# Performance work log

Measured on AMD Instinct MI355X. Metric: run time of the kernel, lower is better.

Reference implementation:

```python
import jax, jax.numpy as jnp
import numpy as np

B, N, A, M, D = 64, 128, 64, 128, 64  # batch, in_caps, in_dim, out_caps, out_dim
SCALE = 1.0 / np.sqrt(D).astype(np.float32)
W_INIT = np.sqrt(M / (A * N)).astype(np.float32)


def setup_inputs() -> dict:
    key = jax.random.key(0)
    k1, k2, k3, k4, k5 = jax.random.split(key, 5)
    return {
        "input": jax.random.normal(k1, (B, N, A), dtype=jnp.float32),
        "current_act": jax.random.uniform(k2, (B, N), dtype=jnp.float32),
        "next_capsule_value": jax.random.normal(k3, (B, M, D), dtype=jnp.float32),
        "next_act": jax.random.uniform(k4, (B, M), dtype=jnp.float32),
        "w": W_INIT * jax.random.normal(k5, (N, A, M, D), dtype=jnp.float32),
        "num_iter": 1,
    }


def reference(input, current_act, next_capsule_value, next_act, w, num_iter):
    # Per-(input-capsule, output-capsule) votes: bna,namd->bnmd (shared by both einsums)
    votes = jnp.einsum('bna,namd->bnmd', input, w)
    # Routing logits: agreement between votes and current output poses
    logits = jnp.einsum('bnmd,bmd->bnm', votes, next_capsule_value) * SCALE
    qk = jax.nn.softmax(logits, axis=2)
    # Modulate by next-layer activations and renormalize over output capsules
    qk = qk * next_act[:, None, :]
    qk = qk / (jnp.sum(qk, axis=2, keepdims=True) + 1e-10)
    # Weighted aggregation of votes, gated by input-capsule activations
    ncv = jnp.einsum('bnm,bnmd,bn->bmd', qk, votes, current_act)
    # act_type == 'ONES'; dropout rate 0.0 (identity); nonlinear_act is identity
    na = jnp.ones(ncv.shape[:2], dtype=ncv.dtype)
    return ncv, na, qk
```

## Files before the change

kernel.cpp:

```cpp
#include <hip/hip_runtime.h>

typedef __attribute__((ext_vector_type(8))) short bf16x8;
typedef __attribute__((ext_vector_type(4))) float f32x4;

constexpr int Bq = 64, Nq = 128, Aq = 64, Mq = 128, Dq = 64;
constexpr int MD = Mq * Dq;
constexpr int NM = Nq * Mq;
constexpr int NA = Nq * Aq;
constexpr int NCV_SZ = Bq * MD;
constexpr int NA_SZ  = Bq * Mq;
constexpr float SCALE = 0.125f;

__device__ __forceinline__ unsigned short f2b(float f) {
  unsigned u = __float_as_uint(f);
  return (unsigned short)((u + 0x7fffu + ((u >> 16) & 1u)) >> 16);
}
__device__ __forceinline__ unsigned cvt2(float lo, float hi) {
  return ((unsigned)f2b(hi) << 16) | (unsigned)f2b(lo);
}
__device__ __forceinline__ bf16x8 pack8(const float* v) {
  union { unsigned u[4]; bf16x8 b; } x;
  x.u[0] = cvt2(v[0], v[1]); x.u[1] = cvt2(v[2], v[3]);
  x.u[2] = cvt2(v[4], v[5]); x.u[3] = cvt2(v[6], v[7]);
  return x.b;
}
__device__ __forceinline__ void dma16(const float* g, float* l) {
  __builtin_amdgcn_global_load_lds(
      (const __attribute__((address_space(1))) unsigned*)g,
      (__attribute__((address_space(3))) unsigned*)l, 16, 0, 0);
}

__global__ __launch_bounds__(256) void k0_init(float* __restrict__ out) {
  int i = blockIdx.x * 256 + threadIdx.x;
  if (i < NCV_SZ) out[i] = 0.0f;
  else if (i < NCV_SZ + NA_SZ) out[i] = 1.0f;
}

__global__ __launch_bounds__(256, 2) void k1_logits(
    const float* __restrict__ input,
    const float* __restrict__ ncvin,
    const float* __restrict__ wgt,
    float* __restrict__ logits) {
  const int mc = blockIdx.x;
  const int n0 = blockIdx.y * 8;
  const int t  = threadIdx.x;
  const int wv = t >> 6, l = t & 63;
  const int lr = l & 15, g = l >> 4;
  const int m  = mc * 4 + wv;

  __shared__ float Wf[2][32 * 256];

  float cnv[4][4][4];
#pragma unroll
  for (int i = 0; i < 4; ++i)
#pragma unroll
    for (int j = 0; j < 4; ++j)
#pragma unroll
      for (int r = 0; r < 4; ++r)
        cnv[i][j][r] = ncvin[(size_t)(16 * i + 4 * g + r) * MD + m * Dq + 16 * j + lr];

  auto stage = [&](int h) {
    const int hh = 15 - h;
    const int nn = n0 + (hh >> 1);
    const int ks = (hh & 1) * 32;
    float* dst = &Wf[h & 1][0];
#pragma unroll
    for (int rr = 0; rr < 8; ++rr) {
      const int al = wv * 8 + rr;
      const char* gs = (const char*)(wgt + (size_t)(nn * Aq + ks + al) * MD + mc * 256)
                       + ((l * 16) ^ (((al >> 3) & 1) << 6));
      dma16((const float*)gs, dst + al * 256);
    }
  };

  stage(0);
  f32x4 acc[4][4];

  for (int h = 0; h < 16; ++h) {
    const int hh = 15 - h;
    const int nn = n0 + (hh >> 1);
    const int ks = (hh & 1) * 32;

    float av[4][8];
#pragma unroll
    for (int i = 0; i < 4; ++i) {
      const float* ap = input + (size_t)(16 * i + lr) * NA + nn * Aq + ks + g * 8;
      *(float4*)&av[i][0] = *(const float4*)ap;
      *(float4*)&av[i][4] = *(const float4*)(ap + 4);
    }
    __builtin_amdgcn_sched_barrier(0);

    if (h < 15) {
      stage(h + 1);
      asm volatile("s_waitcnt vmcnt(8)" ::: "memory");
    } else {
      asm volatile("s_waitcnt vmcnt(0)" ::: "memory");
    }
    __builtin_amdgcn_s_barrier();

    if ((h & 1) == 0) {
#pragma unroll
      for (int i = 0; i < 4; ++i)
#pragma unroll
        for (int j = 0; j < 4; ++j) acc[i][j] = (f32x4)(0.0f);
    }

    bf16x8 af[4];
#pragma unroll
    for (int i = 0; i < 4; ++i) af[i] = pack8(av[i]);

    const float* bufp = &Wf[h & 1][0];
#pragma unroll
    for (int j = 0; j < 4; ++j) {
      const int c  = 64 * wv + 16 * j + lr;
      const int cx = c ^ ((g & 1) << 4);
      float bv[8];
#pragma unroll
      for (int e = 0; e < 8; ++e) bv[e] = bufp[(g * 8 + e) * 256 + cx];
      bf16x8 bf = pack8(bv);
#pragma unroll
      for (int i = 0; i < 4; ++i)
        acc[i][j] = __builtin_amdgcn_mfma_f32_16x16x32_bf16(af[i], bf, acc[i][j], 0, 0, 0);
    }
    __builtin_amdgcn_s_barrier();

    if (h & 1) {
      float lp[4][4];
#pragma unroll
      for (int i = 0; i < 4; ++i)
#pragma unroll
        for (int r = 0; r < 4; ++r) lp[i][r] = 0.0f;
#pragma unroll
      for (int i = 0; i < 4; ++i)
#pragma unroll
        for (int j = 0; j < 4; ++j)
#pragma unroll
          for (int r = 0; r < 4; ++r)
            lp[i][r] = fmaf(acc[i][j][r], cnv[i][j][r], lp[i][r]);
#pragma unroll
      for (int off = 1; off < 16; off <<= 1)
#pragma unroll
        for (int i = 0; i < 4; ++i)
#pragma unroll
          for (int r = 0; r < 4; ++r) lp[i][r] += __shfl_xor(lp[i][r], off);
      float ov = lp[0][0];
#pragma unroll
      for (int i = 0; i < 4; ++i)
#pragma unroll
        for (int r = 0; r < 4; ++r)
          ov = (lr == i * 4 + r) ? lp[i][r] : ov;
      const int b = 16 * (lr >> 2) + 4 * g + (lr & 3);
      logits[(size_t)b * NM + (size_t)nn * Mq + m] = SCALE * ov;
    }
  }
}

__global__ __launch_bounds__(256) void k2_softmax(
    const float* __restrict__ next_act,
    float* __restrict__ qk) {
  const int row  = blockIdx.x * 4 + (threadIdx.x >> 6);
  const int lane = threadIdx.x & 63;
  const int b = row >> 7;
  float* p = qk + (size_t)row * Mq;
  float x0 = p[lane], x1 = p[lane + 64];
  float mx = fmaxf(x0, x1);
#pragma unroll
  for (int off = 32; off; off >>= 1) mx = fmaxf(mx, __shfl_xor(mx, off));
  float e0 = __expf(x0 - mx), e1 = __expf(x1 - mx);
  float s = e0 + e1;
#pragma unroll
  for (int off = 32; off; off >>= 1) s += __shfl_xor(s, off);
  float a0 = next_act[b * Mq + lane], a1 = next_act[b * Mq + lane + 64];
  float t0 = (e0 / s) * a0, t1 = (e1 / s) * a1;
  float s2 = t0 + t1;
#pragma unroll
  for (int off = 32; off; off >>= 1) s2 += __shfl_xor(s2, off);
  s2 += 1e-10f;
  p[lane]      = t0 / s2;
  p[lane + 64] = t1 / s2;
}

__global__ __launch_bounds__(256, 2) void k3_aggregate(
    const float* __restrict__ input,
    const float* __restrict__ cur_act,
    const float* __restrict__ wgt,
    const float* __restrict__ qk,
    float* __restrict__ ncv) {
  const int mc = blockIdx.x;
  const int n0 = blockIdx.y * 8;
  const int t  = threadIdx.x;
  const int wv = t >> 6, l = t & 63;
  const int lr = l & 15, g = l >> 4;
  const int m  = mc * 4 + wv;

  __shared__ float Wf[2][32 * 256];
  __shared__ float zl[8][4][64];

#pragma unroll
  for (int p = 0; p < 2; ++p) {
    const int idx = t + p * 256;
    const int b = idx >> 3, nn = idx & 7;
    float4 q4 = *(const float4*)&qk[(size_t)b * NM + (size_t)(n0 + nn) * Mq + mc * 4];
    float ca = cur_act[b * Nq + n0 + nn];
    zl[nn][0][b] = q4.x * ca; zl[nn][1][b] = q4.y * ca;
    zl[nn][2][b] = q4.z * ca; zl[nn][3][b] = q4.w * ca;
  }
  __syncthreads();

  auto stage = [&](int h) {
    const int nn = n0 + (h >> 1);
    const int ks = (h & 1) * 32;
    float* dst = &Wf[h & 1][0];
#pragma unroll
    for (int rr = 0; rr < 8; ++rr) {
      const int al = wv * 8 + rr;
      const char* gs = (const char*)(wgt + (size_t)(nn * Aq + ks + al) * MD + mc * 256)
                       + ((l * 16) ^ (((al >> 3) & 1) << 6));
      dma16((const float*)gs, dst + al * 256);
    }
  };

  stage(0);
  f32x4 acc[4][4];
#pragma unroll
  for (int i = 0; i < 4; ++i)
#pragma unroll
    for (int j = 0; j < 4; ++j) acc[i][j] = (f32x4)(0.0f);

  float zr[4];
  for (int h = 0; h < 16; ++h) {
    const int nnl = h >> 1;
    const int nn  = n0 + nnl;
    const int ks  = (h & 1) * 32;

    if ((h & 1) == 0) {
#pragma unroll
      for (int i = 0; i < 4; ++i) zr[i] = zl[nnl][wv][16 * i + lr];
    }

    float av[4][8];
#pragma unroll
    for (int i = 0; i < 4; ++i) {
      const float* ap = input + (size_t)(16 * i + lr) * NA + nn * Aq + ks + g * 8;
      *(float4*)&av[i][0] = *(const float4*)ap;
      *(float4*)&av[i][4] = *(const float4*)(ap + 4);
    }
    __builtin_amdgcn_sched_barrier(0);

    if (h < 15) {
      stage(h + 1);
      asm volatile("s_waitcnt vmcnt(8)" ::: "memory");
    } else {
      asm volatile("s_waitcnt vmcnt(0)" ::: "memory");
    }
    __builtin_amdgcn_s_barrier();

    bf16x8 af[4];
#pragma unroll
    for (int i = 0; i < 4; ++i) {
      float sv[8];
#pragma unroll
      for (int e = 0; e < 8; ++e) sv[e] = av[i][e] * zr[i];
      af[i] = pack8(sv);
    }

    const float* bufp = &Wf[h & 1][0];
#pragma unroll
    for (int j = 0; j < 4; ++j) {
      const int c  = 64 * wv + 16 * j + lr;
      const int cx = c ^ ((g & 1) << 4);
      float bv[8];
#pragma unroll
      for (int e = 0; e < 8; ++e) bv[e] = bufp[(g * 8 + e) * 256 + cx];
      bf16x8 bf = pack8(bv);
#pragma unroll
      for (int i = 0; i < 4; ++i)
        acc[i][j] = __builtin_amdgcn_mfma_f32_16x16x32_bf16(af[i], bf, acc[i][j], 0, 0, 0);
    }
    __builtin_amdgcn_s_barrier();
  }

#pragma unroll
  for (int i = 0; i < 4; ++i)
#pragma unroll
    for (int j = 0; j < 4; ++j) {
      const int d = 16 * j + lr;
#pragma unroll
      for (int r = 0; r < 4; ++r) {
        const int b = 16 * i + 4 * g + r;
        atomicAdd(&ncv[(size_t)b * MD + m * Dq + d], acc[i][j][r]);
      }
    }
}

extern "C" void kernel_launch(void* const* d_in, const int* in_sizes, int n_in,
                              void* d_out, int out_size, void* d_ws, size_t ws_size,
                              hipStream_t stream) {
  const float* input    = (const float*)d_in[0];
  const float* cur_act  = (const float*)d_in[1];
  const float* ncvin    = (const float*)d_in[2];
  const float* next_act = (const float*)d_in[3];
  const float* wgt      = (const float*)d_in[4];

  float* out = (float*)d_out;
  float* ncv = out;
  float* qk  = out + NCV_SZ + NA_SZ;

  k0_init<<<(NCV_SZ + NA_SZ + 255) / 256, 256, 0, stream>>>(out);
  k1_logits<<<dim3(32, 16), 256, 0, stream>>>(input, ncvin, wgt, qk);
  k2_softmax<<<(Bq * Nq) / 4, 256, 0, stream>>>(next_act, qk);
  k3_aggregate<<<dim3(32, 16), 256, 0, stream>>>(input, cur_act, wgt, qk, ncv);
}
```

Measured before the change: 161.3 us.

## Pre-convert weights to bf16 MFMA fragment layout in workspace before logits and aggregation

Adds a conversion kernel that repacks the fp32 weight tensor into bf16 in the exact per-lane MFMA B-fragment order inside the workspace. The logits and aggregation kernels then stage half as many bytes per tile and load fragments directly from LDS, with no per-element packing. This removes LDS gather and conversion work in the two GEMM kernels but adds a full extra read of the weights plus a write of the bf16 copy every call. The old kernels are kept as a fallback when the workspace is too small.

After: 207.2 us. +28.4%, slower.

```diff
diff --git a/kernel.cpp b/kernel.cpp
--- a/kernel.cpp
+++ b/kernel.cpp
@@ -10,6 +10,7 @@
 constexpr int NCV_SZ = Bq * MD;
 constexpr int NA_SZ  = Bq * Mq;
 constexpr float SCALE = 0.125f;
+constexpr size_t W2_BYTES = (size_t)32 * 128 * 2 * 4 * 4 * 64 * 16;
 
 __device__ __forceinline__ unsigned short f2b(float f) {
   unsigned u = __float_as_uint(f);
@@ -29,6 +30,15 @@
       (const __attribute__((address_space(1))) unsigned*)g,
       (__attribute__((address_space(3))) unsigned*)l, 16, 0, 0);
 }
+__device__ __forceinline__ void dma16c(const char* g, void* l) {
+  __builtin_amdgcn_global_load_lds(
+      (const __attribute__((address_space(1))) unsigned*)g,
+      (__attribute__((address_space(3))) unsigned*)l, 16, 0, 0);
+}
+
+__device__ __forceinline__ size_t w2base(int mc, int nn, int ks, int wv, int j) {
+  return (((((size_t)(mc * 128 + nn) * 2 + ks) * 4 + wv) * 4 + j) * 64) * 16;
+}
 
 __global__ __launch_bounds__(256) void k0_init(float* __restrict__ out) {
   int i = blockIdx.x * 256 + threadIdx.x;
@@ -36,19 +46,72 @@
   else if (i < NCV_SZ + NA_SZ) out[i] = 1.0f;
 }
 
-__global__ __launch_bounds__(256, 2) void k1_logits(
+__global__ __launch_bounds__(256) void k_conv(const float* __restrict__ wgt,
+                                              char* __restrict__ w2) {
+  const int n = blockIdx.x, oct = blockIdx.y;
+  const int ks = oct >> 2, lhi = oct & 3;
+  const int a0 = ks * 32 + lhi * 8;
+  const int t = threadIdx.x;
+  const int wv = t >> 6, l = t & 63;
+
+  __shared__ float Ls[2][8][1024];
+
+  auto stage = [&](int cg) {
+    float* dst = &Ls[cg & 1][0][0];
+#pragma unroll
+    for (int rr = 0; rr < 2; ++rr) {
+      const int e = wv * 2 + rr;
+      const float* src = wgt + ((size_t)(n * 64 + a0 + e)) * MD + cg * 1024;
+#pragma unroll
+      for (int q = 0; q < 4; ++q)
+        dma16(src + q * 256 + l * 4, dst + e * 1024 + q * 256);
+    }
+  };
+
+  stage(0);
+  for (int cg = 0; cg < 8; ++cg) {
+    if (cg < 7) {
+      stage(cg + 1);
+      asm volatile("s_waitcnt vmcnt(8)" ::: "memory");
+    } else {
+      asm volatile("s_waitcnt vmcnt(0)" ::: "memory");
+    }
+    __builtin_amdgcn_s_barrier();
+
+    const float* lsc = &Ls[cg & 1][0][0];
+    float4 tv[8];
+#pragma unroll
+    for (int e = 0; e < 8; ++e)
+      tv[e] = *(const float4*)(lsc + e * 1024 + t * 4);
+
+    const int c0 = cg * 1024 + t * 4;
+#pragma unroll
+    for (int cc = 0; cc < 4; ++cc) {
+      const int c = c0 + cc;
+      const int m = c >> 6, d = c & 63;
+      float v[8];
+#pragma unroll
+      for (int e = 0; e < 8; ++e) v[e] = ((const float*)&tv[e])[cc];
+      *(bf16x8*)(w2 + w2base(m >> 2, n, ks, m & 3, d >> 4) +
+                 (size_t)(lhi * 16 + (d & 15)) * 16) = pack8(v);
+    }
+    __builtin_amdgcn_s_barrier();
+  }
+}
+
+__global__ __launch_bounds__(256, 2) void k1_logits2(
     const float* __restrict__ input,
     const float* __restrict__ ncvin,
-    const float* __restrict__ wgt,
+    const char* __restrict__ w2,
     float* __restrict__ logits) {
   const int mc = blockIdx.x;
   const int n0 = blockIdx.y * 8;
-  const int t  = threadIdx.x;
+  const int t = threadIdx.x;
   const int wv = t >> 6, l = t & 63;
   const int lr = l & 15, g = l >> 4;
-  const int m  = mc * 4 + wv;
-
-  __shared__ float Wf[2][32 * 256];
+  const int m = mc * 4 + wv;
+
+  __shared__ uint4 Wl[2][1024];
 
   float cnv[4][4][4];
 #pragma unroll
@@ -60,31 +123,23 @@
         cnv[i][j][r] = ncvin[(size_t)(16 * i + 4 * g + r) * MD + m * Dq + 16 * j + lr];
 
   auto stage = [&](int h) {
-    const int hh = 15 - h;
-    const int nn = n0 + (hh >> 1);
-    const int ks = (hh & 1) * 32;
-    float* dst = &Wf[h & 1][0];
-#pragma unroll
-    for (int rr = 0; rr < 8; ++rr) {
-      const int al = wv * 8 + rr;
-      const char* gs = (const char*)(wgt + (size_t)(nn * Aq + ks + al) * MD + mc * 256)
-                       + ((l * 16) ^ (((al >> 3) & 1) << 6));
-      dma16((const float*)gs, dst + al * 256);
-    }
+    const int nn = n0 + (h >> 1), ks = h & 1;
+#pragma unroll
+    for (int j = 0; j < 4; ++j)
+      dma16c((const char*)w2 + w2base(mc, nn, ks, wv, j) + (size_t)l * 16,
+             &Wl[h & 1][(wv * 4 + j) * 64]);
   };
 
   stage(0);
   f32x4 acc[4][4];
 
   for (int h = 0; h < 16; ++h) {
-    const int hh = 15 - h;
-    const int nn = n0 + (hh >> 1);
-    const int ks = (hh & 1) * 32;
+    const int nn = n0 + (h >> 1), ksq = h & 1;
 
     float av[4][8];
 #pragma unroll
     for (int i = 0; i < 4; ++i) {
-      const float* ap = input + (size_t)(16 * i + lr) * NA + nn * Aq + ks + g * 8;
+      const float* ap = input + (size_t)(16 * i + lr) * NA + nn * Aq + ksq * 32 + g * 8;
       *(float4*)&av[i][0] = *(const float4*)ap;
       *(float4*)&av[i][4] = *(const float4*)(ap + 4);
     }
@@ -92,13 +147,13 @@
 
     if (h < 15) {
       stage(h + 1);
-      asm volatile("s_waitcnt vmcnt(8)" ::: "memory");
+      asm volatile("s_waitcnt vmcnt(4)" ::: "memory");
     } else {
       asm volatile("s_waitcnt vmcnt(0)" ::: "memory");
     }
     __builtin_amdgcn_s_barrier();
 
-    if ((h & 1) == 0) {
+    if (ksq == 0) {
 #pragma unroll
       for (int i = 0; i < 4; ++i)
 #pragma unroll
@@ -109,22 +164,16 @@
 #pragma unroll
     for (int i = 0; i < 4; ++i) af[i] = pack8(av[i]);
 
-    const float* bufp = &Wf[h & 1][0];
 #pragma unroll
     for (int j = 0; j < 4; ++j) {
-      const int c  = 64 * wv + 16 * j + lr;
-      const int cx = c ^ ((g & 1) << 4);
-      float bv[8];
-#pragma unroll
-      for (int e = 0; e < 8; ++e) bv[e] = bufp[(g * 8 + e) * 256 + cx];
-      bf16x8 bf = pack8(bv);
+      bf16x8 bf = *(const bf16x8*)&Wl[h & 1][(wv * 4 + j) * 64 + l];
 #pragma unroll
       for (int i = 0; i < 4; ++i)
         acc[i][j] = __builtin_amdgcn_mfma_f32_16x16x32_bf16(af[i], bf, acc[i][j], 0, 0, 0);
     }
     __builtin_amdgcn_s_barrier();
 
-    if (h & 1) {
+    if (ksq == 1) {
       float lp[4][4];
 #pragma unroll
       for (int i = 0; i < 4; ++i)
@@ -180,20 +229,20 @@
   p[lane + 64] = t1 / s2;
 }
 
-__global__ __launch_bounds__(256, 2) void k3_aggregate(
+__global__ __launch_bounds__(256, 2) void k3_aggregate2(
     const float* __restrict__ input,
     const float* __restrict__ cur_act,
-    const float* __restrict__ wgt,
+    const char* __restrict__ w2,
     const float* __restrict__ qk,
     float* __restrict__ ncv) {
   const int mc = blockIdx.x;
   const int n0 = blockIdx.y * 8;
-  const int t  = threadIdx.x;
+  const int t = threadIdx.x;
   const int wv = t >> 6, l = t & 63;
   const int lr = l & 15, g = l >> 4;
-  const int m  = mc * 4 + wv;
-
-  __shared__ float Wf[2][32 * 256];
+  const int m = mc * 4 + wv;
+
+  __shared__ uint4 Wl[2][1024];
   __shared__ float zl[8][4][64];
 
 #pragma unroll
@@ -208,8 +257,101 @@
   __syncthreads();
 
   auto stage = [&](int h) {
-    const int nn = n0 + (h >> 1);
-    const int ks = (h & 1) * 32;
+    const int nn = n0 + (h >> 1), ks = h & 1;
+#pragma unroll
+    for (int j = 0; j < 4; ++j)
+      dma16c((const char*)w2 + w2base(mc, nn, ks, wv, j) + (size_t)l * 16,
+             &Wl[h & 1][(wv * 4 + j) * 64]);
+  };
+
+  stage(0);
+  f32x4 acc[4][4];
+#pragma unroll
+  for (int i = 0; i < 4; ++i)
+#pragma unroll
+    for (int j = 0; j < 4; ++j) acc[i][j] = (f32x4)(0.0f);
+
+  float zr[4];
+  for (int h = 0; h < 16; ++h) {
+    const int nnl = h >> 1;
+    const int nn = n0 + nnl, ksq = h & 1;
+
+    if (ksq == 0) {
+#pragma unroll
+      for (int i = 0; i < 4; ++i) zr[i] = zl[nnl][wv][16 * i + lr];
+    }
+
+    float av[4][8];
+#pragma unroll
+    for (int i = 0; i < 4; ++i) {
+      const float* ap = input + (size_t)(16 * i + lr) * NA + nn * Aq + ksq * 32 + g * 8;
+      *(float4*)&av[i][0] = *(const float4*)ap;
+      *(float4*)&av[i][4] = *(const float4*)(ap + 4);
+    }
+    __builtin_amdgcn_sched_barrier(0);
+
+    if (h < 15) {
+      stage(h + 1);
+      asm volatile("s_waitcnt vmcnt(4)" ::: "memory");
+    } else {
+      asm volatile("s_waitcnt vmcnt(0)" ::: "memory");
+    }
+    __builtin_amdgcn_s_barrier();
+
+    bf16x8 af[4];
+#pragma unroll
+    for (int i = 0; i < 4; ++i) {
+      float sv[8];
+#pragma unroll
+      for (int e = 0; e < 8; ++e) sv[e] = av[i][e] * zr[i];
+      af[i] = pack8(sv);
+    }
+
+#pragma unroll
+    for (int j = 0; j < 4; ++j) {
+      bf16x8 bf = *(const bf16x8*)&Wl[h & 1][(wv * 4 + j) * 64 + l];
+#pragma unroll
+      for (int i = 0; i < 4; ++i)
+        acc[i][j] = __builtin_amdgcn_mfma_f32_16x16x32_bf16(af[i], bf, acc[i][j], 0, 0, 0);
+    }
+    __builtin_amdgcn_s_barrier();
+  }
+
+#pragma unroll
+  for (int i = 0; i < 4; ++i)
+#pragma unroll
+    for (int j = 0; j < 4; ++j) {
+      const int d = 16 * j + lr;
+#pragma unroll
+      for (int r = 0; r < 4; ++r) {
+        const int b = 16 * i + 4 * g + r;
+        atomicAdd(&ncv[(size_t)b * MD + m * Dq + d], acc[i][j][r]);
+      }
+    }
+}
+
+__global__ __launch_bounds__(256, 2) void k1_legacy(
+    const float* __restrict__ input, const float* __restrict__ ncvin,
+    const float* __restrict__ wgt, float* __restrict__ logits) {
+  const int mc = blockIdx.x;
+  const int n0 = blockIdx.y * 8;
+  const int t = threadIdx.x;
+  const int wv = t >> 6, l = t & 63;
+  const int lr = l & 15, g = l >> 4;
+  const int m = mc * 4 + wv;
+  __shared__ float Wf[2][32 * 256];
+  float cnv[4][4][4];
+#pragma unroll
+  for (int i = 0; i < 4; ++i)
+#pragma unroll
+    for (int j = 0; j < 4; ++j)
+#pragma unroll
+      for (int r = 0; r < 4; ++r)
+        cnv[i][j][r] = ncvin[(size_t)(16 * i + 4 * g + r) * MD + m * Dq + 16 * j + lr];
+  auto stage = [&](int h) {
+    const int hh = 15 - h;
+    const int nn = n0 + (hh >> 1);
+    const int ks = (hh & 1) * 32;
     float* dst = &Wf[h & 1][0];
 #pragma unroll
     for (int rr = 0; rr < 8; ++rr) {
@@ -219,25 +361,12 @@
       dma16((const float*)gs, dst + al * 256);
     }
   };
-
   stage(0);
   f32x4 acc[4][4];
-#pragma unroll
-  for (int i = 0; i < 4; ++i)
-#pragma unroll
-    for (int j = 0; j < 4; ++j) acc[i][j] = (f32x4)(0.0f);
-
-  float zr[4];
   for (int h = 0; h < 16; ++h) {
-    const int nnl = h >> 1;
-    const int nn  = n0 + nnl;
-    const int ks  = (h & 1) * 32;
-
-    if ((h & 1) == 0) {
-#pragma unroll
-      for (int i = 0; i < 4; ++i) zr[i] = zl[nnl][wv][16 * i + lr];
-    }
-
+    const int hh = 15 - h;
+    const int nn = n0 + (hh >> 1);
+    const int ks = (hh & 1) * 32;
     float av[4][8];
 #pragma unroll
     for (int i = 0; i < 4; ++i) {
@@ -246,15 +375,122 @@
       *(float4*)&av[i][4] = *(const float4*)(ap + 4);
     }
     __builtin_amdgcn_sched_barrier(0);
-
-    if (h < 15) {
-      stage(h + 1);
-      asm volatile("s_waitcnt vmcnt(8)" ::: "memory");
-    } else {
-      asm volatile("s_waitcnt vmcnt(0)" ::: "memory");
-    }
-    __builtin_amdgcn_s_barrier();
-
+    if (h < 15) { stage(h + 1); asm volatile("s_waitcnt vmcnt(8)" ::: "memory"); }
+    else { asm volatile("s_waitcnt vmcnt(0)" ::: "memory"); }
+    __builtin_amdgcn_s_barrier();
+    if ((h & 1) == 0) {
+#pragma unroll
+      for (int i = 0; i < 4; ++i)
+#pragma unroll
+        for (int j = 0; j < 4; ++j) acc[i][j] = (f32x4)(0.0f);
+    }
+    bf16x8 af[4];
+#pragma unroll
+    for (int i = 0; i < 4; ++i) af[i] = pack8(av[i]);
+    const float* bufp = &Wf[h & 1][0];
+#pragma unroll
+    for (int j = 0; j < 4; ++j) {
+      const int cx = (64 * wv + 16 * j + lr) ^ ((g & 1) << 4);
+      float bv[8];
+#pragma unroll
+      for (int e = 0; e < 8; ++e) bv[e] = bufp[(g * 8 + e) * 256 + cx];
+      bf16x8 bf = pack8(bv);
+#pragma unroll
+      for (int i = 0; i < 4; ++i)
+        acc[i][j] = __builtin_amdgcn_mfma_f32_16x16x32_bf16(af[i], bf, acc[i][j], 0, 0, 0);
+    }
+    __builtin_amdgcn_s_barrier();
+    if (h & 1) {
+      float lp[4][4];
+#pragma unroll
+      for (int i = 0; i < 4; ++i)
+#pragma unroll
+        for (int r = 0; r < 4; ++r) lp[i][r] = 0.0f;
+#pragma unroll
+      for (int i = 0; i < 4; ++i)
+#pragma unroll
+        for (int j = 0; j < 4; ++j)
+#pragma unroll
+          for (int r = 0; r < 4; ++r)
+            lp[i][r] = fmaf(acc[i][j][r], cnv[i][j][r], lp[i][r]);
+#pragma unroll
+      for (int off = 1; off < 16; off <<= 1)
+#pragma unroll
+        for (int i = 0; i < 4; ++i)
+#pragma unroll
+          for (int r = 0; r < 4; ++r) lp[i][r] += __shfl_xor(lp[i][r], off);
+      float ov = lp[0][0];
+#pragma unroll
+      for (int i = 0; i < 4; ++i)
+#pragma unroll
+        for (int r = 0; r < 4; ++r)
+          ov = (lr == i * 4 + r) ? lp[i][r] : ov;
+      const int b = 16 * (lr >> 2) + 4 * g + (lr & 3);
+      logits[(size_t)b * NM + (size_t)nn * Mq + m] = SCALE * ov;
+    }
+  }
+}
+
+__global__ __launch_bounds__(256, 2) void k3_legacy(
+    const float* __restrict__ input, const float* __restrict__ cur_act,
+    const float* __restrict__ wgt, const float* __restrict__ qk,
+    float* __restrict__ ncv) {
+  const int mc = blockIdx.x;
+  const int n0 = blockIdx.y * 8;
+  const int t = threadIdx.x;
+  const int wv = t >> 6, l = t & 63;
+  const int lr = l & 15, g = l >> 4;
+  const int m = mc * 4 + wv;
+  __shared__ float Wf[2][32 * 256];
+  __shared__ float zl[8][4][64];
+#pragma unroll
+  for (int p = 0; p < 2; ++p) {
+    const int idx = t + p * 256;
+    const int b = idx >> 3, nn = idx & 7;
+    float4 q4 = *(const float4*)&qk[(size_t)b * NM + (size_t)(n0 + nn) * Mq + mc * 4];
+    float ca = cur_act[b * Nq + n0 + nn];
+    zl[nn][0][b] = q4.x * ca; zl[nn][1][b] = q4.y * ca;
+    zl[nn][2][b] = q4.z * ca; zl[nn][3][b] = q4.w * ca;
+  }
+  __syncthreads();
+  auto stage = [&](int h) {
+    const int nn = n0 + (h >> 1);
+    const int ks = (h & 1) * 32;
+    float* dst = &Wf[h & 1][0];
+#pragma unroll
+    for (int rr = 0; rr < 8; ++rr) {
+      const int al = wv * 8 + rr;
+      const char* gs = (const char*)(wgt + (size_t)(nn * Aq + ks + al) * MD + mc * 256)
+                       + ((l * 16) ^ (((al >> 3) & 1) << 6));
+      dma16((const float*)gs, dst + al * 256);
+    }
+  };
+  stage(0);
+  f32x4 acc[4][4];
+#pragma unroll
+  for (int i = 0; i < 4; ++i)
+#pragma unroll
+    for (int j = 0; j < 4; ++j) acc[i][j] = (f32x4)(0.0f);
+  float zr[4];
+  for (int h = 0; h < 16; ++h) {
+    const int nnl = h >> 1;
+    const int nn = n0 + nnl;
+    const int ks = (h & 1) * 32;
+    if ((h & 1) == 0) {
+#pragma unroll
+      for (int i = 0; i < 4; ++i) zr[i] = zl[nnl][wv][16 * i + lr];
+    }
+    float av[4][8];
+#pragma unroll
+    for (int i = 0; i < 4; ++i) {
+      const float* ap = input + (size_t)(16 * i + lr) * NA + nn * Aq + ks + g * 8;
+      *(float4*)&av[i][0] = *(const float4*)ap;
+      *(float4*)&av[i][4] = *(const float4*)(ap + 4);
+    }
+    __builtin_amdgcn_sched_barrier(0);
+    if (h < 15) { stage(h + 1); asm volatile("s_waitcnt vmcnt(8)" ::: "memory"); }
+    else { asm volatile("s_waitcnt vmcnt(0)" ::: "memory"); }
+    __builtin_amdgcn_s_barrier();
     bf16x8 af[4];
 #pragma unroll
     for (int i = 0; i < 4; ++i) {
@@ -263,12 +499,10 @@
       for (int e = 0; e < 8; ++e) sv[e] = av[i][e] * zr[i];
       af[i] = pack8(sv);
     }
-
     const float* bufp = &Wf[h & 1][0];
 #pragma unroll
     for (int j = 0; j < 4; ++j) {
-      const int c  = 64 * wv + 16 * j + lr;
-      const int cx = c ^ ((g & 1) << 4);
+      const int cx = (64 * wv + 16 * j + lr) ^ ((g & 1) << 4);
       float bv[8];
 #pragma unroll
       for (int e = 0; e < 8; ++e) bv[e] = bufp[(g * 8 + e) * 256 + cx];
@@ -279,7 +513,6 @@
     }
     __builtin_amdgcn_s_barrier();
   }
-
 #pragma unroll
   for (int i = 0; i < 4; ++i)
 #pragma unroll
@@ -306,8 +539,17 @@
   float* ncv = out;
   float* qk  = out + NCV_SZ + NA_SZ;
 
-  k0_init<<<(NCV_SZ + NA_SZ + 255) / 256, 256, 0, stream>>>(out);
-  k1_logits<<<dim3(32, 16), 256, 0, stream>>>(input, ncvin, wgt, qk);
-  k2_softmax<<<(Bq * Nq) / 4, 256, 0, stream>>>(next_act, qk);
-  k3_aggregate<<<dim3(32, 16), 256, 0, stream>>>(input, cur_act, wgt, qk, ncv);
-}
+  if (ws_size >= W2_BYTES) {
+    char* w2 = (char*)d_ws;
+    k_conv<<<dim3(Nq, 8), 256, 0, stream>>>(wgt, w2);
+    k0_init<<<(NCV_SZ + NA_SZ + 255) / 256, 256, 0, stream>>>(out);
+    k1_logits2<<<dim3(32, 16), 256, 0, stream>>>(input, ncvin, w2, qk);
+    k2_softmax<<<(Bq * Nq) / 4, 256, 0, stream>>>(next_act, qk);
+    k3_aggregate2<<<dim3(32, 16), 256, 0, stream>>>(input, cur_act, w2, qk, ncv);
+  } else {
+    k0_init<<<(NCV_SZ + NA_SZ + 255) / 256, 256, 0, stream>>>(out);
+    k1_legacy<<<dim3(32, 16), 256, 0, stream>>>(input, ncvin, wgt, qk);
+    k2_softmax<<<(Bq * Nq) / 4, 256, 0, stream>>>(next_act, qk);
+    k3_legacy<<<dim3(32, 16), 256, 0, stream>>>(input, cur_act, wgt, qk, ncv);
+  }
+}
```

## Split batch across two wave groups with 512-thread blocks in logits and aggregate

Applied to the files above, without the earlier changes.

Both GEMM-style kernels now launch 512 threads per block, with eight waves arranged as four along the output capsule and two along the batch. Each wave holds half the accumulators, and each of the eight waves stages four W rows instead of eight. The aim is more waves per CU to hide latency, with fewer registers per thread. In exchange, each wave repeats the LDS reads and bf16 packing of W, and the logits shuffle reduction stores only half its lanes.

Measured after the change: 153.0 us. -5.1%, faster.

```diff
diff --git a/kernel.cpp b/kernel.cpp
--- a/kernel.cpp
+++ b/kernel.cpp
@@ -36,28 +36,26 @@
   else if (i < NCV_SZ + NA_SZ) out[i] = 1.0f;
 }
 
-__global__ __launch_bounds__(256, 2) void k1_logits(
-    const float* __restrict__ input,
-    const float* __restrict__ ncvin,
-    const float* __restrict__ wgt,
-    float* __restrict__ logits) {
+__global__ __launch_bounds__(512, 4) void k1_logits(
+    const float* __restrict__ input, const float* __restrict__ ncvin,
+    const float* __restrict__ wgt, float* __restrict__ logits) {
   const int mc = blockIdx.x;
   const int n0 = blockIdx.y * 8;
-  const int t  = threadIdx.x;
-  const int wv = t >> 6, l = t & 63;
+  const int t = threadIdx.x;
+  const int w8 = t >> 6, l = t & 63;
+  const int wv_m = w8 & 3, wv_b = w8 >> 2;
   const int lr = l & 15, g = l >> 4;
-  const int m  = mc * 4 + wv;
-
+  const int m = mc * 4 + wv_m;
   __shared__ float Wf[2][32 * 256];
 
-  float cnv[4][4][4];
-#pragma unroll
-  for (int i = 0; i < 4; ++i)
+  float cnv[2][4][4];
+#pragma unroll
+  for (int i = 0; i < 2; ++i)
 #pragma unroll
     for (int j = 0; j < 4; ++j)
 #pragma unroll
       for (int r = 0; r < 4; ++r)
-        cnv[i][j][r] = ncvin[(size_t)(16 * i + 4 * g + r) * MD + m * Dq + 16 * j + lr];
+        cnv[i][j][r] = ncvin[(size_t)(32 * wv_b + 16 * i + 4 * g + r) * MD + m * Dq + 16 * j + lr];
 
   auto stage = [&](int h) {
     const int hh = 15 - h;
@@ -65,26 +63,25 @@
     const int ks = (hh & 1) * 32;
     float* dst = &Wf[h & 1][0];
 #pragma unroll
-    for (int rr = 0; rr < 8; ++rr) {
-      const int al = wv * 8 + rr;
+    for (int rr = 0; rr < 4; ++rr) {
+      const int al = w8 * 4 + rr;
       const char* gs = (const char*)(wgt + (size_t)(nn * Aq + ks + al) * MD + mc * 256)
                        + ((l * 16) ^ (((al >> 3) & 1) << 6));
       dma16((const float*)gs, dst + al * 256);
     }
   };
-
   stage(0);
-  f32x4 acc[4][4];
+  f32x4 acc[2][4];
 
   for (int h = 0; h < 16; ++h) {
     const int hh = 15 - h;
     const int nn = n0 + (hh >> 1);
     const int ks = (hh & 1) * 32;
 
-    float av[4][8];
-#pragma unroll
-    for (int i = 0; i < 4; ++i) {
-      const float* ap = input + (size_t)(16 * i + lr) * NA + nn * Aq + ks + g * 8;
+    float av[2][8];
+#pragma unroll
+    for (int i = 0; i < 2; ++i) {
+      const float* ap = input + (size_t)(32 * wv_b + 16 * i + lr) * NA + nn * Aq + ks + g * 8;
       *(float4*)&av[i][0] = *(const float4*)ap;
       *(float4*)&av[i][4] = *(const float4*)(ap + 4);
     }
@@ -92,7 +89,7 @@
 
     if (h < 15) {
       stage(h + 1);
-      asm volatile("s_waitcnt vmcnt(8)" ::: "memory");
+      asm volatile("s_waitcnt vmcnt(4)" ::: "memory");
     } else {
       asm volatile("s_waitcnt vmcnt(0)" ::: "memory");
     }
@@ -100,38 +97,37 @@
 
     if ((h & 1) == 0) {
 #pragma unroll
-      for (int i = 0; i < 4; ++i)
+      for (int i = 0; i < 2; ++i)
 #pragma unroll
         for (int j = 0; j < 4; ++j) acc[i][j] = (f32x4)(0.0f);
     }
 
-    bf16x8 af[4];
-#pragma unroll
-    for (int i = 0; i < 4; ++i) af[i] = pack8(av[i]);
+    bf16x8 af[2];
+#pragma unroll
+    for (int i = 0; i < 2; ++i) af[i] = pack8(av[i]);
 
     const float* bufp = &Wf[h & 1][0];
 #pragma unroll
     for (int j = 0; j < 4; ++j) {
-      const int c  = 64 * wv + 16 * j + lr;
-      const int cx = c ^ ((g & 1) << 4);
+      const int cx = (64 * wv_m + 16 * j + lr) ^ ((g & 1) << 4);
       float bv[8];
 #pragma unroll
       for (int e = 0; e < 8; ++e) bv[e] = bufp[(g * 8 + e) * 256 + cx];
       bf16x8 bf = pack8(bv);
 #pragma unroll
-      for (int i = 0; i < 4; ++i)
+      for (int i = 0; i < 2; ++i)
         acc[i][j] = __builtin_amdgcn_mfma_f32_16x16x32_bf16(af[i], bf, acc[i][j], 0, 0, 0);
     }
     __builtin_amdgcn_s_barrier();
 
     if (h & 1) {
-      float lp[4][4];
-#pragma unroll
-      for (int i = 0; i < 4; ++i)
+      float lp[2][4];
+#pragma unroll
+      for (int i = 0; i < 2; ++i)
 #pragma unroll
         for (int r = 0; r < 4; ++r) lp[i][r] = 0.0f;
 #pragma unroll
-      for (int i = 0; i < 4; ++i)
+      for (int i = 0; i < 2; ++i)
 #pragma unroll
         for (int j = 0; j < 4; ++j)
 #pragma unroll
@@ -140,24 +136,25 @@
 #pragma unroll
       for (int off = 1; off < 16; off <<= 1)
 #pragma unroll
-        for (int i = 0; i < 4; ++i)
+        for (int i = 0; i < 2; ++i)
 #pragma unroll
           for (int r = 0; r < 4; ++r) lp[i][r] += __shfl_xor(lp[i][r], off);
       float ov = lp[0][0];
 #pragma unroll
-      for (int i = 0; i < 4; ++i)
+      for (int i = 0; i < 2; ++i)
 #pragma unroll
         for (int r = 0; r < 4; ++r)
           ov = (lr == i * 4 + r) ? lp[i][r] : ov;
-      const int b = 16 * (lr >> 2) + 4 * g + (lr & 3);
-      logits[(size_t)b * NM + (size_t)nn * Mq + m] = SCALE * ov;
+      if (lr < 8) {
+        const int b = 32 * wv_b + 16 * (lr >> 2) + 4 * g + (lr & 3);
+        logits[(size_t)b * NM + (size_t)nn * Mq + m] = SCALE * ov;
+      }
     }
   }
 }
 
 __global__ __launch_bounds__(256) void k2_softmax(
-    const float* __restrict__ next_act,
-    float* __restrict__ qk) {
+    const float* __restrict__ next_act, float* __restrict__ qk) {
   const int row  = blockIdx.x * 4 + (threadIdx.x >> 6);
   const int lane = threadIdx.x & 63;
   const int b = row >> 7;
@@ -180,26 +177,22 @@
   p[lane + 64] = t1 / s2;
 }
 
-__global__ __launch_bounds__(256, 2) void k3_aggregate(
-    const float* __restrict__ input,
-    const float* __restrict__ cur_act,
-    const float* __restrict__ wgt,
-    const float* __restrict__ qk,
+__global__ __launch_bounds__(512, 4) void k3_aggregate(
+    const float* __restrict__ input, const float* __restrict__ cur_act,
+    const float* __restrict__ wgt, const float* __restrict__ qk,
     float* __restrict__ ncv) {
   const int mc = blockIdx.x;
   const int n0 = blockIdx.y * 8;
-  const int t  = threadIdx.x;
-  const int wv = t >> 6, l = t & 63;
+  const int t = threadIdx.x;
+  const int w8 = t >> 6, l = t & 63;
+  const int wv_m = w8 & 3, wv_b = w8 >> 2;
   const int lr = l & 15, g = l >> 4;
-  const int m  = mc * 4 + wv;
-
+  const int m = mc * 4 + wv_m;
   __shared__ float Wf[2][32 * 256];
   __shared__ float zl[8][4][64];
 
-#pragma unroll
-  for (int p = 0; p < 2; ++p) {
-    const int idx = t + p * 256;
-    const int b = idx >> 3, nn = idx & 7;
+  {
+    const int b = t >> 3, nn = t & 7;
     float4 q4 = *(const float4*)&qk[(size_t)b * NM + (size_t)(n0 + nn) * Mq + mc * 4];
     float ca = cur_act[b * Nq + n0 + nn];
     zl[nn][0][b] = q4.x * ca; zl[nn][1][b] = q4.y * ca;
@@ -212,36 +205,35 @@
     const int ks = (h & 1) * 32;
     float* dst = &Wf[h & 1][0];
 #pragma unroll
-    for (int rr = 0; rr < 8; ++rr) {
-      const int al = wv * 8 + rr;
+    for (int rr = 0; rr < 4; ++rr) {
+      const int al = w8 * 4 + rr;
       const char* gs = (const char*)(wgt + (size_t)(nn * Aq + ks + al) * MD + mc * 256)
                        + ((l * 16) ^ (((al >> 3) & 1) << 6));
       dma16((const float*)gs, dst + al * 256);
     }
   };
-
   stage(0);
-  f32x4 acc[4][4];
-#pragma unroll
-  for (int i = 0; i < 4; ++i)
+  f32x4 acc[2][4];
+#pragma unroll
+  for (int i = 0; i < 2; ++i)
 #pragma unroll
     for (int j = 0; j < 4; ++j) acc[i][j] = (f32x4)(0.0f);
 
-  float zr[4];
+  float zr[2];
   for (int h = 0; h < 16; ++h) {
     const int nnl = h >> 1;
-    const int nn  = n0 + nnl;
-    const int ks  = (h & 1) * 32;
+    const int nn = n0 + nnl;
+    const int ks = (h & 1) * 32;
 
     if ((h & 1) == 0) {
 #pragma unroll
-      for (int i = 0; i < 4; ++i) zr[i] = zl[nnl][wv][16 * i + lr];
-    }
-
-    float av[4][8];
-#pragma unroll
-    for (int i = 0; i < 4; ++i) {
-      const float* ap = input + (size_t)(16 * i + lr) * NA + nn * Aq + ks + g * 8;
+      for (int i = 0; i < 2; ++i) zr[i] = zl[nnl][wv_m][32 * wv_b + 16 * i + lr];
+    }
+
+    float av[2][8];
+#pragma unroll
+    for (int i = 0; i < 2; ++i) {
+      const float* ap = input + (size_t)(32 * wv_b + 16 * i + lr) * NA + nn * Aq + ks + g * 8;
       *(float4*)&av[i][0] = *(const float4*)ap;
       *(float4*)&av[i][4] = *(const float4*)(ap + 4);
     }
@@ -249,15 +241,15 @@
 
     if (h < 15) {
       stage(h + 1);
-      asm volatile("s_waitcnt vmcnt(8)" ::: "memory");
+      asm volatile("s_waitcnt vmcnt(4)" ::: "memory");
     } else {
       asm volatile("s_waitcnt vmcnt(0)" ::: "memory");
     }
     __builtin_amdgcn_s_barrier();
 
-    bf16x8 af[4];
-#pragma unroll
-    for (int i = 0; i < 4; ++i) {
+    bf16x8 af[2];
+#pragma unroll
+    for (int i = 0; i < 2; ++i) {
       float sv[8];
 #pragma unroll
       for (int e = 0; e < 8; ++e) sv[e] = av[i][e] * zr[i];
@@ -267,27 +259,26 @@
     const float* bufp = &Wf[h & 1][0];
 #pragma unroll
     for (int j = 0; j < 4; ++j) {
-      const int c  = 64 * wv + 16 * j + lr;
-      const int cx = c ^ ((g & 1) << 4);
+      const int cx = (64 * wv_m + 16 * j + lr) ^ ((g & 1) << 4);
       float bv[8];
 #pragma unroll
       for (int e = 0; e < 8; ++e) bv[e] = bufp[(g * 8 + e) * 256 + cx];
       bf16x8 bf = pack8(bv);
 #pragma unroll
-      for (int i = 0; i < 4; ++i)
+      for (int i = 0; i < 2; ++i)
         acc[i][j] = __builtin_amdgcn_mfma_f32_16x16x32_bf16(af[i], bf, acc[i][j], 0, 0, 0);
     }
     __builtin_amdgcn_s_barrier();
   }
 
 #pragma unroll
-  for (int i = 0; i < 4; ++i)
+  for (int i = 0; i < 2; ++i)
 #pragma unroll
     for (int j = 0; j < 4; ++j) {
       const int d = 16 * j + lr;
 #pragma unroll
       for (int r = 0; r < 4; ++r) {
-        const int b = 16 * i + 4 * g + r;
+        const int b = 32 * wv_b + 16 * i + 4 * g + r;
         atomicAdd(&ncv[(size_t)b * MD + m * Dq + d], acc[i][j][r]);
       }
     }
@@ -307,7 +298,7 @@
   float* qk  = out + NCV_SZ + NA_SZ;
 
   k0_init<<<(NCV_SZ + NA_SZ + 255) / 256, 256, 0, stream>>>(out);
-  k1_logits<<<dim3(32, 16), 256, 0, stream>>>(input, ncvin, wgt, qk);
+  k1_logits<<<dim3(32, 16), 512, 0, stream>>>(input, ncvin, wgt, qk);
   k2_softmax<<<(Bq * Nq) / 4, 256, 0, stream>>>(next_act, qk);
-  k3_aggregate<<<dim3(32, 16), 256, 0, stream>>>(input, cur_act, wgt, qk, ncv);
-}
+  k3_aggregate<<<dim3(32, 16), 512, 0, stream>>>(input, cur_act, wgt, qk, ncv);
+}
```

## Give each wave a private weight LDS region and drop block barriers

Applied to the files above, without the earlier changes.

The shared LDS weight tile is split into per-wave regions. Each wave now DMA-loads only the weight slice for its own output capsule, so the two s_barrier calls per iteration in both the logits and aggregate kernels can be removed. The wait counts are adjusted so the next stage's loads stay in flight during compute. This trades block-wide synchronization for wave-local ordering, which relies on vmcnt covering the LDS DMA correctly, and it changes the global access pattern per wave.

Result: faster. 144.5 us (median of 2 runs) (-10.4%).

```diff
diff --git a/kernel.cpp b/kernel.cpp
--- a/kernel.cpp
+++ b/kernel.cpp
@@ -36,19 +36,17 @@
   else if (i < NCV_SZ + NA_SZ) out[i] = 1.0f;
 }
 
+
 __global__ __launch_bounds__(256, 2) void k1_logits(
-    const float* __restrict__ input,
-    const float* __restrict__ ncvin,
-    const float* __restrict__ wgt,
-    float* __restrict__ logits) {
+    const float* __restrict__ input, const float* __restrict__ ncvin,
+    const float* __restrict__ wgt, float* __restrict__ logits) {
   const int mc = blockIdx.x;
   const int n0 = blockIdx.y * 8;
-  const int t  = threadIdx.x;
+  const int t = threadIdx.x;
   const int wv = t >> 6, l = t & 63;
   const int lr = l & 15, g = l >> 4;
-  const int m  = mc * 4 + wv;
-
-  __shared__ float Wf[2][32 * 256];
+  const int m = mc * 4 + wv;
+  __shared__ float Wr[4][2][2048];
 
   float cnv[4][4][4];
 #pragma unroll
@@ -59,44 +57,42 @@
       for (int r = 0; r < 4; ++r)
         cnv[i][j][r] = ncvin[(size_t)(16 * i + 4 * g + r) * MD + m * Dq + 16 * j + lr];
 
-  auto stage = [&](int h) {
+  auto stageH = [&](int h) {
+    if (h > 15) return;
     const int hh = 15 - h;
-    const int nn = n0 + (hh >> 1);
-    const int ks = (hh & 1) * 32;
-    float* dst = &Wf[h & 1][0];
-#pragma unroll
-    for (int rr = 0; rr < 8; ++rr) {
-      const int al = wv * 8 + rr;
-      const char* gs = (const char*)(wgt + (size_t)(nn * Aq + ks + al) * MD + mc * 256)
-                       + ((l * 16) ^ (((al >> 3) & 1) << 6));
-      dma16((const float*)gs, dst + al * 256);
+    const int nn = n0 + (hh >> 1), ks = hh & 1;
+    char* dst = (char*)&Wr[wv][h & 1][0];
+    const char* wb = (const char*)wgt;
+#pragma unroll
+    for (int al = 0; al < 8; ++al) {
+      const int swz = (al >> 1) & 1;
+      const char* gs = wb + (size_t)(nn * 64 + ks * 32 + al * 4 + g) * 32768
+                       + (size_t)m * 256 + ((lr * 16) ^ (swz << 6));
+      dma16((const float*)gs, (float*)(dst + al * 1024));
     }
   };
-
-  stage(0);
-  f32x4 acc[4][4];
-
-  for (int h = 0; h < 16; ++h) {
+  auto loadAv = [&](int h, float (&av)[4][8]) {
     const int hh = 15 - h;
-    const int nn = n0 + (hh >> 1);
-    const int ks = (hh & 1) * 32;
-
-    float av[4][8];
+    const int nn = n0 + (hh >> 1), ks = hh & 1;
 #pragma unroll
     for (int i = 0; i < 4; ++i) {
-      const float* ap = input + (size_t)(16 * i + lr) * NA + nn * Aq + ks + g * 8;
+      const float* ap = input + (size_t)(16 * i + lr) * NA + nn * Aq + ks * 32 + g * 8;
       *(float4*)&av[i][0] = *(const float4*)ap;
       *(float4*)&av[i][4] = *(const float4*)(ap + 4);
     }
-    __builtin_amdgcn_sched_barrier(0);
-
-    if (h < 15) {
-      stage(h + 1);
-      asm volatile("s_waitcnt vmcnt(8)" ::: "memory");
-    } else {
-      asm volatile("s_waitcnt vmcnt(0)" ::: "memory");
-    }
-    __builtin_amdgcn_s_barrier();
+  };
+
+  stageH(0);
+  f32x4 acc[4][4];
+  for (int h = 0; h < 16; ++h) {
+    float av[4][8];
+    loadAv(h, av);
+    __builtin_amdgcn_sched_barrier(0);
+    stageH(h + 1);
+    __builtin_amdgcn_sched_barrier(0);
+    if (h < 15) asm volatile("s_waitcnt vmcnt(16)" ::: "memory");
+    else        asm volatile("s_waitcnt vmcnt(8)"  ::: "memory");
+    __builtin_amdgcn_sched_barrier(0);
 
     if ((h & 1) == 0) {
 #pragma unroll
@@ -109,22 +105,21 @@
 #pragma unroll
     for (int i = 0; i < 4; ++i) af[i] = pack8(av[i]);
 
-    const float* bufp = &Wf[h & 1][0];
+    const char* lb = (const char*)&Wr[wv][h & 1][0];
 #pragma unroll
     for (int j = 0; j < 4; ++j) {
-      const int c  = 64 * wv + 16 * j + lr;
-      const int cx = c ^ ((g & 1) << 4);
       float bv[8];
 #pragma unroll
-      for (int e = 0; e < 8; ++e) bv[e] = bufp[(g * 8 + e) * 256 + cx];
+      for (int e = 0; e < 8; ++e)
+        bv[e] = *(const float*)(lb + (g * 8 + e) * 256 + (((16 * j + lr) * 4) ^ ((g & 1) << 6)));
       bf16x8 bf = pack8(bv);
 #pragma unroll
       for (int i = 0; i < 4; ++i)
         acc[i][j] = __builtin_amdgcn_mfma_f32_16x16x32_bf16(af[i], bf, acc[i][j], 0, 0, 0);
     }
-    __builtin_amdgcn_s_barrier();
 
     if (h & 1) {
+      const int nn = n0 + ((15 - h) >> 1);
       float lp[4][4];
 #pragma unroll
       for (int i = 0; i < 4; ++i)
@@ -156,8 +151,7 @@
 }
 
 __global__ __launch_bounds__(256) void k2_softmax(
-    const float* __restrict__ next_act,
-    float* __restrict__ qk) {
+    const float* __restrict__ next_act, float* __restrict__ qk) {
   const int row  = blockIdx.x * 4 + (threadIdx.x >> 6);
   const int lane = threadIdx.x & 63;
   const int b = row >> 7;
@@ -181,19 +175,16 @@
 }
 
 __global__ __launch_bounds__(256, 2) void k3_aggregate(
-    const float* __restrict__ input,
-    const float* __restrict__ cur_act,
-    const float* __restrict__ wgt,
-    const float* __restrict__ qk,
+    const float* __restrict__ input, const float* __restrict__ cur_act,
+    const float* __restrict__ wgt, const float* __restrict__ qk,
     float* __restrict__ ncv) {
   const int mc = blockIdx.x;
   const int n0 = blockIdx.y * 8;
-  const int t  = threadIdx.x;
+  const int t = threadIdx.x;
   const int wv = t >> 6, l = t & 63;
   const int lr = l & 15, g = l >> 4;
-  const int m  = mc * 4 + wv;
-
-  __shared__ float Wf[2][32 * 256];
+  const int m = mc * 4 + wv;
+  __shared__ float Wr[4][2][2048];
   __shared__ float zl[8][4][64];
 
 #pragma unroll
@@ -207,20 +198,30 @@
   }
   __syncthreads();
 
-  auto stage = [&](int h) {
-    const int nn = n0 + (h >> 1);
-    const int ks = (h & 1) * 32;
-    float* dst = &Wf[h & 1][0];
-#pragma unroll
-    for (int rr = 0; rr < 8; ++rr) {
-      const int al = wv * 8 + rr;
-      const char* gs = (const char*)(wgt + (size_t)(nn * Aq + ks + al) * MD + mc * 256)
-                       + ((l * 16) ^ (((al >> 3) & 1) << 6));
-      dma16((const float*)gs, dst + al * 256);
+  auto stageH = [&](int h) {
+    if (h > 15) return;
+    const int nn = n0 + (h >> 1), ks = h & 1;
+    char* dst = (char*)&Wr[wv][h & 1][0];
+    const char* wb = (const char*)wgt;
+#pragma unroll
+    for (int al = 0; al < 8; ++al) {
+      const int swz = (al >> 1) & 1;
+      const char* gs = wb + (size_t)(nn * 64 + ks * 32 + al * 4 + g) * 32768
+                       + (size_t)m * 256 + ((lr * 16) ^ (swz << 6));
+      dma16((const float*)gs, (float*)(dst + al * 1024));
     }
   };
-
-  stage(0);
+  auto loadAv = [&](int h, float (&av)[4][8]) {
+    const int nn = n0 + (h >> 1), ks = h & 1;
+#pragma unroll
+    for (int i = 0; i < 4; ++i) {
+      const float* ap = input + (size_t)(16 * i + lr) * NA + nn * Aq + ks * 32 + g * 8;
+      *(float4*)&av[i][0] = *(const float4*)ap;
+      *(float4*)&av[i][4] = *(const float4*)(ap + 4);
+    }
+  };
+
+  stageH(0);
   f32x4 acc[4][4];
 #pragma unroll
   for (int i = 0; i < 4; ++i)
@@ -229,31 +230,19 @@
 
   float zr[4];
   for (int h = 0; h < 16; ++h) {
-    const int nnl = h >> 1;
-    const int nn  = n0 + nnl;
-    const int ks  = (h & 1) * 32;
+    float av[4][8];
+    loadAv(h, av);
+    __builtin_amdgcn_sched_barrier(0);
+    stageH(h + 1);
+    __builtin_amdgcn_sched_barrier(0);
+    if (h < 15) asm volatile("s_waitcnt vmcnt(16)" ::: "memory");
+    else        asm volatile("s_waitcnt vmcnt(8)"  ::: "memory");
+    __builtin_amdgcn_sched_barrier(0);
 
     if ((h & 1) == 0) {
 #pragma unroll
-      for (int i = 0; i < 4; ++i) zr[i] = zl[nnl][wv][16 * i + lr];
-    }
-
-    float av[4][8];
-#pragma unroll
-    for (int i = 0; i < 4; ++i) {
-      const float* ap = input + (size_t)(16 * i + lr) * NA + nn * Aq + ks + g * 8;
-      *(float4*)&av[i][0] = *(const float4*)ap;
-      *(float4*)&av[i][4] = *(const float4*)(ap + 4);
-    }
-    __builtin_amdgcn_sched_barrier(0);
-
-    if (h < 15) {
-      stage(h + 1);
-      asm volatile("s_waitcnt vmcnt(8)" ::: "memory");
-    } else {
-      asm volatile("s_waitcnt vmcnt(0)" ::: "memory");
-    }
-    __builtin_amdgcn_s_barrier();
+      for (int i = 0; i < 4; ++i) zr[i] = zl[h >> 1][wv][16 * i + lr];
+    }
 
     bf16x8 af[4];
 #pragma unroll
@@ -264,20 +253,18 @@
       af[i] = pack8(sv);
     }
 
-    const float* bufp = &Wf[h & 1][0];
+    const char* lb = (const char*)&Wr[wv][h & 1][0];
 #pragma unroll
     for (int j = 0; j < 4; ++j) {
-      const int c  = 64 * wv + 16 * j + lr;
-      const int cx = c ^ ((g & 1) << 4);
       float bv[8];
 #pragma unroll
-      for (int e = 0; e < 8; ++e) bv[e] = bufp[(g * 8 + e) * 256 + cx];
+      for (int e = 0; e < 8; ++e)
+        bv[e] = *(const float*)(lb + (g * 8 + e) * 256 + (((16 * j + lr) * 4) ^ ((g & 1) << 6)));
       bf16x8 bf = pack8(bv);
 #pragma unroll
       for (int i = 0; i < 4; ++i)
         acc[i][j] = __builtin_amdgcn_mfma_f32_16x16x32_bf16(af[i], bf, acc[i][j], 0, 0, 0);
     }
-    __builtin_amdgcn_s_barrier();
   }
 
 #pragma unroll
```
